# Kernel tuning notes

Hardware: AMD Instinct MI355X
Metric: run time of the kernel (lower is better)

The kernel has to match this reference:

```python
import jax, jax.numpy as jnp
import numpy as np

B, L, H, HEADS = 4, 2048, 512, 8
D = H // HEADS  # 64


def setup_inputs() -> dict:
    key = jax.random.key(0)
    ks = jax.random.split(key, 13)
    s = 0.02
    return {
        "q_in": jax.random.normal(ks[0], (B, L, H), jnp.float32),
        "k_in": jax.random.normal(ks[1], (B, L, H), jnp.float32),
        "v_in": jax.random.normal(ks[2], (B, L, H), jnp.float32),
        "Wq_w": jax.random.normal(ks[3], (H, H), jnp.float32) * s,
        "Wq_b": jax.random.normal(ks[4], (H,), jnp.float32) * s,
        "Wk_w": jax.random.normal(ks[5], (H, H), jnp.float32) * s,
        "Wk_b": jax.random.normal(ks[6], (H,), jnp.float32) * s,
        "Wv_w": jax.random.normal(ks[7], (H, H), jnp.float32) * s,
        "Wv_b": jax.random.normal(ks[8], (H,), jnp.float32) * s,
        "Wo_w": jax.random.normal(ks[9], (H, H), jnp.float32) * s,
        "Wo_b": jax.random.normal(ks[10], (H,), jnp.float32) * s,
        "Wp_w": jax.random.normal(ks[11], (2 * L - 1, D), jnp.float32) * s,
        "Wp_b": jax.random.normal(ks[12], (2 * L - 1,), jnp.float32) * s,
    }


def _skew(p):
    # p: (b, h, l, 2l-1) -> relative-position bias (b, h, l, l) via pad/flatten/reshape skew trick
    b, h, l, _ = p.shape
    p = jnp.pad(p, ((0, 0), (0, 0), (0, 0), (0, 1)))          # (b,h,l,2l)
    p = p.reshape(b, h, 2 * l * l)
    p = jnp.pad(p, ((0, 0), (0, 0), (0, l - 1)))               # (b,h,(l+1)(2l-1))
    p = p.reshape(b, h, l + 1, 2 * l - 1)
    return p[:, :, :-1, -l:]                                   # (b,h,l,l)


def reference(q_in, k_in, v_in, Wq_w, Wq_b, Wk_w, Wk_b, Wv_w, Wv_b, Wo_w, Wo_b, Wp_w, Wp_b):
    b, l, hid = q_in.shape
    q = q_in @ Wq_w.T + Wq_b
    k = k_in @ Wk_w.T + Wk_b
    v = v_in @ Wv_w.T + Wv_b
    # (b, l, h*d) -> (b, h, l, d)
    to_heads = lambda x: x.reshape(b, l, HEADS, D).transpose(0, 2, 1, 3)
    q, k, v = to_heads(q), to_heads(k), to_heads(v)
    q = q / jnp.sqrt(jnp.asarray(D, q.dtype))  # scaling applied BEFORE posenc, as in original
    scores = jnp.einsum('bhid,bhjd->bhij', q, k)
    pos = _skew(q @ Wp_w.T + Wp_b)             # posenc linear applied to scaled q
    scores = scores + pos
    attn = jax.nn.softmax(scores, axis=-1)     # (b,h,l,l)
    # Original torch.einsum('b h l l, b h l d -> b h l d') takes the DIAGONAL of attn
    diag = jnp.diagonal(attn, axis1=-2, axis2=-1)  # (b,h,l)
    out = diag[..., None] * v                       # (b,h,l,d)
    out = out.transpose(0, 2, 1, 3).reshape(b, l, hid)
    return out @ Wo_w.T + Wo_b
```

## Files before the change

### kernel.cpp

```cpp
#include <hip/hip_runtime.h>
#include <cstdint>


typedef unsigned short u16;
typedef __bf16 bf16x8 __attribute__((ext_vector_type(8)));
typedef __bf16 bf16x2 __attribute__((ext_vector_type(2)));
typedef float  f32x16 __attribute__((ext_vector_type(16)));
typedef uint32_t __attribute__((address_space(1))) as1_u32;
typedef uint32_t __attribute__((address_space(3))) as3_u32;

__device__ __forceinline__ u16 f2bf(float f) {
  __bf16 h = (__bf16)f;
  return __builtin_bit_cast(u16, h);
}
__device__ __forceinline__ uint32_t pkbf(float a, float b) {
  bf16x2 v; v[0] = (__bf16)a; v[1] = (__bf16)b;
  return __builtin_bit_cast(uint32_t, v);
}
__device__ __forceinline__ float bf2f(u16 u) {
  return __uint_as_float(((uint32_t)u) << 16);
}
__device__ __forceinline__ float exp2v(float x) {
  float r;
  asm("v_exp_f32 %0, %1" : "=v"(r) : "v"(x));
  return r;
}
__device__ __forceinline__ void gl_lds16(const void* g, void* l) {
  __builtin_amdgcn_global_load_lds((const as1_u32*)g, (as3_u32*)l, 16, 0, 0);
}

__global__ __launch_bounds__(256) void prep_kernel(
    const float* __restrict__ qin, const float* __restrict__ kin, const float* __restrict__ vin,
    const float* __restrict__ wq,  const float* __restrict__ wk,  const float* __restrict__ wv,
    const float* __restrict__ wo,  const float* __restrict__ wp,
    u16* __restrict__ xq, u16* __restrict__ xk, u16* __restrict__ xv,
    u16* __restrict__ bwq, u16* __restrict__ bwk, u16* __restrict__ bwv,
    u16* __restrict__ bwo, u16* __restrict__ bwp) {
  long u = (long)blockIdx.x * 256 + threadIdx.x;
  const float* src; u16* dst; long off; float qs = 1.0f;
  if      (u < 524288L)  { src = qin; dst = xq;  off = u; }
  else if (u < 1048576L) { src = kin; dst = xk;  off = u - 524288L; }
  else if (u < 1572864L) { src = vin; dst = xv;  off = u - 1048576L; }
  else if (u < 1605632L) { src = wq;  dst = bwq; off = u - 1572864L; qs = 0.18033688f; }
  else if (u < 1638400L) { src = wk;  dst = bwk; off = u - 1605632L; }
  else if (u < 1671168L) { src = wv;  dst = bwv; off = u - 1638400L; }
  else if (u < 1703936L) { src = wo;  dst = bwo; off = u - 1671168L; }
  else if (u < 1736696L) { src = wp;  dst = bwp; off = u - 1703936L; }
  else {
    long o = (u - 1736696L) * 8 + 262080L;
    uint4 z = {0u, 0u, 0u, 0u};
    *(uint4*)(bwp + o) = z;
    return;
  }
  const float4* s4 = (const float4*)(src + off * 8);
  float4 a = s4[0], b = s4[1];
  uint32_t p0 = pkbf(a.x * qs, a.y * qs);
  uint32_t p1 = pkbf(a.z * qs, a.w * qs);
  uint32_t p2 = pkbf(b.x * qs, b.y * qs);
  uint32_t p3 = pkbf(b.z * qs, b.w * qs);
  uint4 o = {p0, p1, p2, p3};
  *(uint4*)(dst + off * 8) = o;
}

__device__ __forceinline__ void gemm64_core(
    const u16* __restrict__ A, const u16* __restrict__ W, int m0, int n0,
    u16* Al, u16* Bl, int tid, f32x16& acc) {
  const int lane = tid & 63, w = tid >> 6;
  const int wi = w >> 1, wj = w & 1;
  const int l31 = lane & 31, lh = lane >> 5;
  const int r = tid >> 2, ch = tid & 3;
  const int gch = ch ^ ((r >> 1) & 3);
  for (int kb = 0; kb < 16; ++kb) {
    gl_lds16(A + (long)(m0 + r) * 512 + kb * 32 + gch * 8, (char*)Al + w * 64 * 16);
    gl_lds16(W + (long)(n0 + r) * 512 + kb * 32 + gch * 8, (char*)Bl + w * 64 * 16);
    __syncthreads();
    bf16x8 af[2], bfr[2];
#pragma unroll
    for (int ks = 0; ks < 2; ++ks) {
      int c2 = 2 * ks + lh;
      int rA = 32 * wi + l31;
      int rB = 32 * wj + l31;
      af[ks]  = *(const bf16x8*)((char*)Al + (rA * 4 + (c2 ^ ((rA >> 1) & 3))) * 16);
      bfr[ks] = *(const bf16x8*)((char*)Bl + (rB * 4 + (c2 ^ ((rB >> 1) & 3))) * 16);
    }
#pragma unroll
    for (int ks = 0; ks < 2; ++ks)
      acc = __builtin_amdgcn_mfma_f32_32x32x16_bf16(af[ks], bfr[ks], acc, 0, 0, 0);
    __syncthreads();
  }
}

__global__ __launch_bounds__(256, 4) void gemm_bt(
    const u16* __restrict__ A, const u16* __restrict__ W, const float* __restrict__ bias,
    float* __restrict__ ofp) {
  __shared__ u16 Al[64 * 32];
  __shared__ u16 Bl[64 * 32];
  const int tid = threadIdx.x;
  const int lane = tid & 63, w = tid >> 6;
  const int wi = w >> 1, wj = w & 1;
  const int l31 = lane & 31, lh = lane >> 5;
  const int u = (blockIdx.x & 7) * 128 + (blockIdx.x >> 3);
  const int m0 = (u >> 3) * 64, n0 = (u & 7) * 64;

  float bv = bias[n0 + 32 * wj + l31];
  f32x16 acc;
#pragma unroll
  for (int rr = 0; rr < 16; ++rr) acc[rr] = bv;

  gemm64_core(A, W, m0, n0, Al, Bl, tid, acc);

  int n = n0 + 32 * wj + l31;
#pragma unroll
  for (int rr = 0; rr < 16; ++rr) {
    int row = m0 + 32 * wi + (rr & 3) + 8 * (rr >> 2) + 4 * lh;
    ofp[(long)row * 512 + n] = acc[rr];
  }
}

__global__ __launch_bounds__(256, 4) void qkv_gemm(
    const u16* __restrict__ xq, const u16* __restrict__ xk, const u16* __restrict__ xv,
    const u16* __restrict__ wqp, const u16* __restrict__ wkp, const u16* __restrict__ wvp,
    const float* __restrict__ bq, const float* __restrict__ bk, const float* __restrict__ bv,
    u16* __restrict__ oq, u16* __restrict__ ok, u16* __restrict__ ov) {
  __shared__ u16 Al[64 * 32];
  __shared__ u16 Bl[64 * 32];
  const int mat = blockIdx.x >> 10;
  const int t = blockIdx.x & 1023;
  const u16* A = (mat == 0) ? xq : (mat == 1) ? xk : xv;
  const u16* W = (mat == 0) ? wqp : (mat == 1) ? wkp : wvp;
  const float* bias = (mat == 0) ? bq : (mat == 1) ? bk : bv;
  u16* obf = (mat == 0) ? oq : (mat == 1) ? ok : ov;
  const float bsc = (mat == 0) ? 0.18033688f : 1.0f;

  const int tid = threadIdx.x;
  const int lane = tid & 63, w = tid >> 6;
  const int wi = w >> 1, wj = w & 1;
  const int l31 = lane & 31, lh = lane >> 5;
  const int u = (t & 7) * 128 + (t >> 3);
  const int m0 = (u >> 3) * 64, n0 = (u & 7) * 64;

  float bvv = bias[n0 + 32 * wj + l31] * bsc;
  f32x16 acc;
#pragma unroll
  for (int rr = 0; rr < 16; ++rr) acc[rr] = bvv;

  gemm64_core(A, W, m0, n0, Al, Bl, tid, acc);

  int n = n0 + 32 * wj + l31;
  int h = n >> 6, d = n & 63;
#pragma unroll
  for (int rr = 0; rr < 16; ++rr) {
    int row = m0 + 32 * wi + (rr & 3) + 8 * (rr >> 2) + 4 * lh;
    int b = row >> 11, l = row & 2047;
    obf[(((long)(b * 8 + h)) * 2048 + l) * 64 + d] = f2bf(acc[rr]);
  }
}

#define LOADK(T, K0, K1, K2, K3)                                                 \
  do {                                                                           \
    const u16* kp_ = kb + (long)(c0 + 32 * (T) + l31) * 64 + lh * 8;             \
    K0 = *(const bf16x8*)(kp_);                                                  \
    K1 = *(const bf16x8*)(kp_ + 16);                                             \
    K2 = *(const bf16x8*)(kp_ + 32);                                             \
    K3 = *(const bf16x8*)(kp_ + 48);                                             \
  } while (0)

#define LOADNB(M, N0, N1, N2, N3, NV)                                            \
  do {                                                                           \
    int wr_ = wbA + 32 * (M) + l31;                                              \
    const u16* bp_ = wpw + (long)wr_ * 64 + lh * 8;                              \
    N0 = *(const bf16x8*)(bp_);                                                  \
    N1 = *(const bf16x8*)(bp_ + 16);                                             \
    N2 = *(const bf16x8*)(bp_ + 32);                                             \
    N3 = *(const bf16x8*)(bp_ + 48);                                             \
    NV = wpb[wr_ > 4094 ? 4094 : wr_] * 1.44269504f;                             \
  } while (0)

#define PCOMP(RING, G, AQ0, AQ1, AQ2, AQ3, B0, B1, B2, B3, BV)                   \
  do {                                                                           \
    f32x16 accP;                                                                 \
    _Pragma("unroll")                                                            \
    for (int r = 0; r < 16; ++r) accP[r] = (BV);                                 \
    accP = __builtin_amdgcn_mfma_f32_32x32x16_bf16(AQ0, B0, accP, 0, 0, 0);      \
    accP = __builtin_amdgcn_mfma_f32_32x32x16_bf16(AQ1, B1, accP, 0, 0, 0);      \
    accP = __builtin_amdgcn_mfma_f32_32x32x16_bf16(AQ2, B2, accP, 0, 0, 0);      \
    accP = __builtin_amdgcn_mfma_f32_32x32x16_bf16(AQ3, B3, accP, 0, 0, 0);      \
    int bw_ = 32 * (G) + l31 + 4 * lh;                                           \
    _Pragma("unroll")                                                            \
    for (int r = 0; r < 16; ++r) {                                               \
      const int lrr = (r & 3) + 8 * (r >> 2);                                    \
      int uu = (bw_ + lrr) & 127;                                                \
      (RING)[uu * 38 + lrr + 4 * lh] = f2bf(accP[r]);                            \
    }                                                                            \
  } while (0)

#define GATH(RING, T, ACC)                                                       \
  do {                                                                           \
    int u_ = (31 + l31 + 32 * (T)) & 127;                                        \
    const uint32_t* p_ = (const uint32_t*)((RING) + u_ * 38 + 4 * lh);           \
    uint32_t g0 = p_[0], g1 = p_[1], g2 = p_[4],  g3 = p_[5];                    \
    uint32_t g4 = p_[8], g5 = p_[9], g6 = p_[12], g7 = p_[13];                   \
    ACC[0]  = __uint_as_float(g0 << 16); ACC[1]  = __uint_as_float(g0 & 0xffff0000u); \
    ACC[2]  = __uint_as_float(g1 << 16); ACC[3]  = __uint_as_float(g1 & 0xffff0000u); \
    ACC[4]  = __uint_as_float(g2 << 16); ACC[5]  = __uint_as_float(g2 & 0xffff0000u); \
    ACC[6]  = __uint_as_float(g3 << 16); ACC[7]  = __uint_as_float(g3 & 0xffff0000u); \
    ACC[8]  = __uint_as_float(g4 << 16); ACC[9]  = __uint_as_float(g4 & 0xffff0000u); \
    ACC[10] = __uint_as_float(g5 << 16); ACC[11] = __uint_as_float(g5 & 0xffff0000u); \
    ACC[12] = __uint_as_float(g6 << 16); ACC[13] = __uint_as_float(g6 & 0xffff0000u); \
    ACC[14] = __uint_as_float(g7 << 16); ACC[15] = __uint_as_float(g7 & 0xffff0000u); \
  } while (0)

#define ATTN_STEP(T, KC0, KC1, KC2, KC3, KN0, KN1, KN2, KN3,                     \
                  NU0, NU1, NU2, NU3, NUV, NN0, NN1, NN2, NN3, NNV,              \
                  DOK, DOP)                                                      \
  do {                                                                           \
    const int t_ = (T);                                                          \
    if (DOK) { LOADK(t_ + 1, KN0, KN1, KN2, KN3); }                              \
    if (DOP) { LOADNB(t_ + 2, NN0, NN1, NN2, NN3, NNV); }                        \
    accSA = __builtin_amdgcn_mfma_f32_32x32x16_bf16(aqA0, KC0, accSA, 0, 0, 0);  \
    accSA = __builtin_amdgcn_mfma_f32_32x32x16_bf16(aqA1, KC1, accSA, 0, 0, 0);  \
    accSA = __builtin_amdgcn_mfma_f32_32x32x16_bf16(aqA2, KC2, accSA, 0, 0, 0);  \
    accSA = __builtin_amdgcn_mfma_f32_32x32x16_bf16(aqA3, KC3, accSA, 0, 0, 0);  \
    accSB = __builtin_amdgcn_mfma_f32_32x32x16_bf16(aqB0, KC0, accSB, 0, 0, 0);  \
    accSB = __builtin_amdgcn_mfma_f32_32x32x16_bf16(aqB1, KC1, accSB, 0, 0, 0);  \
    accSB = __builtin_amdgcn_mfma_f32_32x32x16_bf16(aqB2, KC2, accSB, 0, 0, 0);  \
    accSB = __builtin_amdgcn_mfma_f32_32x32x16_bf16(aqB3, KC3, accSB, 0, 0, 0);  \
    if (diagw && t_ == tdA) {                                                    \
      _Pragma("unroll")                                                          \
      for (int r = 0; r < 16; ++r) {                                             \
        const int lrr = (r & 3) + 8 * (r >> 2);                                  \
        if (l31 == lrr + 4 * lh) sdiag[lrr + 4 * lh] = accSA[r];                 \
      }                                                                          \
    }                                                                            \
    if (diagw && t_ == tdA + 1) {                                                \
      _Pragma("unroll")                                                          \
      for (int r = 0; r < 16; ++r) {                                             \
        const int lrr = (r & 3) + 8 * (r >> 2);                                  \
        if (l31 == lrr + 4 * lh) sdiag[32 + lrr + 4 * lh] = accSB[r];            \
      }                                                                          \
    }                                                                            \
    _Pragma("unroll")                                                            \
    for (int r = 0; r < 16; ++r) rsum[r] += exp2v(accSA[r]);                     \
    _Pragma("unroll")                                                            \
    for (int r = 0; r < 16; ++r) rsum[16 + r] += exp2v(accSB[r]);                \
    if (DOP) {                                                                   \
      PCOMP(ringB, t_ + 2, aqB0, aqB1, aqB2, aqB3, NU0, NU1, NU2, NU3, NUV);     \
      PCOMP(ringA, t_ + 2, aqA0, aqA1, aqA2, aqA3, NN0, NN1, NN2, NN3, NNV);     \
      GATH(ringA, t_ + 1, accSA);                                                \
      GATH(ringB, t_ + 1, accSB);                                                \
    }                                                                            \
  } while (0)

__global__ __launch_bounds__(256, 2) void attn_kernel(
    const u16* __restrict__ qw, const u16* __restrict__ kw, const u16* __restrict__ vw,
    const u16* __restrict__ wpw, const float* __restrict__ wpb, u16* __restrict__ outp) {
  __shared__ u16 Pl[8 * 128 * 38];
  __shared__ float sdiag[64];
  __shared__ float rssum[64 * 4];
  __shared__ float attw[64];

  const int tid = threadIdx.x, lane = tid & 63, w = tid >> 6;
  const int sbi = blockIdx.x;
  const int x = sbi & 7, g = sbi >> 3;
  const int bh = x + 8 * (g >> 5);
  const int it = g & 31;
  const int i0 = it * 64;
  const u16* qb = qw + (long)bh * 2048 * 64;
  const u16* kb = kw + (long)bh * 2048 * 64;
  const u16* vb = vw + (long)bh * 2048 * 64;

  const int l31 = lane & 31, lh = lane >> 5;
  const int c0 = w << 9;
  const int wbA = 2016 + c0 - i0;
  const bool diagw = (w == (it >> 3));
  const int tdA = 2 * (it & 7);

  u16* ringA = Pl + w * 9728;
  u16* ringB = ringA + 4864;

  bf16x8 aqA0, aqA1, aqA2, aqA3, aqB0, aqB1, aqB2, aqB3;
  {
    const u16* pA = qb + (long)(i0 + l31) * 64 + lh * 8;
    aqA0 = *(const bf16x8*)(pA);
    aqA1 = *(const bf16x8*)(pA + 16);
    aqA2 = *(const bf16x8*)(pA + 32);
    aqA3 = *(const bf16x8*)(pA + 48);
    const u16* pB = pA + 32 * 64;
    aqB0 = *(const bf16x8*)(pB);
    aqB1 = *(const bf16x8*)(pB + 16);
    aqB2 = *(const bf16x8*)(pB + 32);
    aqB3 = *(const bf16x8*)(pB + 48);
  }

  float rsum[32];
#pragma unroll
  for (int r = 0; r < 32; ++r) rsum[r] = 0.f;

  bf16x8 kfA0, kfA1, kfA2, kfA3, kfB0, kfB1, kfB2, kfB3;
  bf16x8 nb00, nb01, nb02, nb03, nb10, nb11, nb12, nb13;
  float nbv0, nbv1;
  f32x16 accSA, accSB;

  {
    bf16x8 t0, t1, t2, t3; float tv;
    LOADNB(-1, t0, t1, t2, t3, tv);
    PCOMP(ringB, 0, aqB0, aqB1, aqB2, aqB3, t0, t1, t2, t3, tv);
    LOADNB(0, t0, t1, t2, t3, tv);
    PCOMP(ringA, 0, aqA0, aqA1, aqA2, aqA3, t0, t1, t2, t3, tv);
    PCOMP(ringB, 1, aqB0, aqB1, aqB2, aqB3, t0, t1, t2, t3, tv);
    LOADNB(1, nb10, nb11, nb12, nb13, nbv1);
    PCOMP(ringA, 1, aqA0, aqA1, aqA2, aqA3, nb10, nb11, nb12, nb13, nbv1);
    LOADK(0, kfA0, kfA1, kfA2, kfA3);
    GATH(ringA, 0, accSA);
    GATH(ringB, 0, accSB);
  }

  for (int tt = 0; tt < 14; tt += 2) {
    ATTN_STEP(tt,     kfA0, kfA1, kfA2, kfA3, kfB0, kfB1, kfB2, kfB3,
              nb10, nb11, nb12, nb13, nbv1, nb00, nb01, nb02, nb03, nbv0,
              true, true);
    ATTN_STEP(tt + 1, kfB0, kfB1, kfB2, kfB3, kfA0, kfA1, kfA2, kfA3,
              nb00, nb01, nb02, nb03, nbv0, nb10, nb11, nb12, nb13, nbv1,
              true, true);
  }
  ATTN_STEP(14, kfA0, kfA1, kfA2, kfA3, kfB0, kfB1, kfB2, kfB3,
            nb10, nb11, nb12, nb13, nbv1, nb00, nb01, nb02, nb03, nbv0,
            true, true);
  ATTN_STEP(15, kfB0, kfB1, kfB2, kfB3, kfA0, kfA1, kfA2, kfA3,
            nb00, nb01, nb02, nb03, nbv0, nb10, nb11, nb12, nb13, nbv1,
            false, false);

#pragma unroll
  for (int r = 0; r < 32; ++r) {
    float v = rsum[r];
    v += __shfl_xor(v, 1);
    v += __shfl_xor(v, 2);
    v += __shfl_xor(v, 4);
    v += __shfl_xor(v, 8);
    v += __shfl_xor(v, 16);
    rsum[r] = v;
  }
  if (l31 == 0) {
#pragma unroll
    for (int r = 0; r < 16; ++r) {
      int lr = (r & 3) + 8 * (r >> 2) + 4 * lh;
      rssum[lr * 4 + w] = rsum[r];
      rssum[(32 + lr) * 4 + w] = rsum[16 + r];
    }
  }
  __syncthreads();
  if (tid < 64) {
    float S = rssum[tid * 4] + rssum[tid * 4 + 1] + rssum[tid * 4 + 2] + rssum[tid * 4 + 3];
    attw[tid] = exp2v(sdiag[tid]) / S;
  }
  __syncthreads();
  {
    int r = tid >> 2, dd = (tid & 3) * 16;
    float a = attw[r];
    int b = bh >> 3, h = bh & 7;
    const u16* vp = vb + (long)(i0 + r) * 64 + dd;
    u16* op = outp + ((long)(b * 2048 + i0 + r)) * 512 + h * 64 + dd;
    uint4 v0 = *(const uint4*)vp;
    uint4 v1 = *(const uint4*)(vp + 8);
    uint32_t vin[8] = {v0.x, v0.y, v0.z, v0.w, v1.x, v1.y, v1.z, v1.w};
    uint32_t vout[8];
#pragma unroll
    for (int e = 0; e < 8; ++e) {
      float lo = bf2f((u16)(vin[e] & 0xffffu)) * a;
      float hi = bf2f((u16)(vin[e] >> 16)) * a;
      vout[e] = pkbf(lo, hi);
    }
    uint4 o0 = {vout[0], vout[1], vout[2], vout[3]};
    uint4 o1 = {vout[4], vout[5], vout[6], vout[7]};
    *(uint4*)op = o0;
    *(uint4*)(op + 8) = o1;
  }
}

extern "C" void kernel_launch(void* const* d_in, const int* in_sizes, int n_in,
                              void* d_out, int out_size, void* d_ws, size_t ws_size,
                              hipStream_t stream) {
  (void)in_sizes; (void)n_in; (void)out_size; (void)ws_size;
  const float* q_in = (const float*)d_in[0];
  const float* k_in = (const float*)d_in[1];
  const float* v_in = (const float*)d_in[2];
  const float* Wq_w = (const float*)d_in[3];
  const float* Wq_b = (const float*)d_in[4];
  const float* Wk_w = (const float*)d_in[5];
  const float* Wk_b = (const float*)d_in[6];
  const float* Wv_w = (const float*)d_in[7];
  const float* Wv_b = (const float*)d_in[8];
  const float* Wo_w = (const float*)d_in[9];
  const float* Wo_b = (const float*)d_in[10];
  const float* Wp_w = (const float*)d_in[11];
  const float* Wp_b = (const float*)d_in[12];

  char* ws = (char*)d_ws;
  u16* xq    = (u16*)(ws + 0);
  u16* xk    = (u16*)(ws + 8388608);
  u16* xv    = (u16*)(ws + 16777216);
  u16* wq    = (u16*)(ws + 25165824);
  u16* wk    = (u16*)(ws + 25690112);
  u16* wv    = (u16*)(ws + 26214400);
  u16* wo    = (u16*)(ws + 26738688);
  u16* wp    = (u16*)(ws + 27262976);
  u16* q_ws  = (u16*)(ws + 27787264);
  u16* k_ws  = (u16*)(ws + 36175872);
  u16* v_ws  = (u16*)(ws + 44564480);
  u16* opre  = (u16*)(ws + 52953088);

  prep_kernel<<<6784, 256, 0, stream>>>(q_in, k_in, v_in, Wq_w, Wk_w, Wv_w, Wo_w, Wp_w,
                                        xq, xk, xv, wq, wk, wv, wo, wp);
  qkv_gemm<<<3072, 256, 0, stream>>>(xq, xk, xv, wq, wk, wv, Wq_b, Wk_b, Wv_b,
                                     q_ws, k_ws, v_ws);
  attn_kernel<<<1024, 256, 0, stream>>>(q_ws, k_ws, v_ws, wp, Wp_b, opre);
  gemm_bt<<<1024, 256, 0, stream>>>(opre, wo, Wo_b, (float*)d_out);
}
```

Baseline: 229.6 us.

## Deepen attention positional-bias pipeline and load GEMM operands directly from global

The attention loop now computes the positional-bias tiles three steps ahead instead of two. The ring gather is split into an early LDS load and a later unpack, so the LDS reads overlap the exp/sum work of the next step. Separately, the projection GEMMs drop the LDS staging and the two barriers per k-step, and each wave loads its bf16 fragments straight from global memory in a fully unrolled loop. This trades barrier and LDS overhead for redundant global traffic across waves and higher register pressure from the deeper prefetch.

Result: slower. 305.7 us (+33.2%).

```diff
diff --git a/kernel.cpp b/kernel.cpp
--- a/kernel.cpp
+++ b/kernel.cpp
@@ -24,9 +24,6 @@
   float r;
   asm("v_exp_f32 %0, %1" : "=v"(r) : "v"(x));
   return r;
-}
-__device__ __forceinline__ void gl_lds16(const void* g, void* l) {
-  __builtin_amdgcn_global_load_lds((const as1_u32*)g, (as3_u32*)l, 16, 0, 0);
 }
 
 __global__ __launch_bounds__(256) void prep_kernel(
@@ -62,39 +59,25 @@
   *(uint4*)(dst + off * 8) = o;
 }
 
-__device__ __forceinline__ void gemm64_core(
+__device__ __forceinline__ void gemm64_direct(
     const u16* __restrict__ A, const u16* __restrict__ W, int m0, int n0,
-    u16* Al, u16* Bl, int tid, f32x16& acc) {
-  const int lane = tid & 63, w = tid >> 6;
-  const int wi = w >> 1, wj = w & 1;
-  const int l31 = lane & 31, lh = lane >> 5;
-  const int r = tid >> 2, ch = tid & 3;
-  const int gch = ch ^ ((r >> 1) & 3);
+    int wi, int wj, int l31, int lh, f32x16& acc) {
+  const u16* Ap = A + (long)(m0 + 32 * wi + l31) * 512 + lh * 8;
+  const u16* Wp = W + (long)(n0 + 32 * wj + l31) * 512 + lh * 8;
+#pragma unroll
   for (int kb = 0; kb < 16; ++kb) {
-    gl_lds16(A + (long)(m0 + r) * 512 + kb * 32 + gch * 8, (char*)Al + w * 64 * 16);
-    gl_lds16(W + (long)(n0 + r) * 512 + kb * 32 + gch * 8, (char*)Bl + w * 64 * 16);
-    __syncthreads();
-    bf16x8 af[2], bfr[2];
-#pragma unroll
-    for (int ks = 0; ks < 2; ++ks) {
-      int c2 = 2 * ks + lh;
-      int rA = 32 * wi + l31;
-      int rB = 32 * wj + l31;
-      af[ks]  = *(const bf16x8*)((char*)Al + (rA * 4 + (c2 ^ ((rA >> 1) & 3))) * 16);
-      bfr[ks] = *(const bf16x8*)((char*)Bl + (rB * 4 + (c2 ^ ((rB >> 1) & 3))) * 16);
-    }
-#pragma unroll
-    for (int ks = 0; ks < 2; ++ks)
-      acc = __builtin_amdgcn_mfma_f32_32x32x16_bf16(af[ks], bfr[ks], acc, 0, 0, 0);
-    __syncthreads();
+    bf16x8 a0 = *(const bf16x8*)(Ap + kb * 32);
+    bf16x8 a1 = *(const bf16x8*)(Ap + kb * 32 + 16);
+    bf16x8 b0 = *(const bf16x8*)(Wp + kb * 32);
+    bf16x8 b1 = *(const bf16x8*)(Wp + kb * 32 + 16);
+    acc = __builtin_amdgcn_mfma_f32_32x32x16_bf16(a0, b0, acc, 0, 0, 0);
+    acc = __builtin_amdgcn_mfma_f32_32x32x16_bf16(a1, b1, acc, 0, 0, 0);
   }
 }
 
 __global__ __launch_bounds__(256, 4) void gemm_bt(
     const u16* __restrict__ A, const u16* __restrict__ W, const float* __restrict__ bias,
     float* __restrict__ ofp) {
-  __shared__ u16 Al[64 * 32];
-  __shared__ u16 Bl[64 * 32];
   const int tid = threadIdx.x;
   const int lane = tid & 63, w = tid >> 6;
   const int wi = w >> 1, wj = w & 1;
@@ -107,7 +90,7 @@
 #pragma unroll
   for (int rr = 0; rr < 16; ++rr) acc[rr] = bv;
 
-  gemm64_core(A, W, m0, n0, Al, Bl, tid, acc);
+  gemm64_direct(A, W, m0, n0, wi, wj, l31, lh, acc);
 
   int n = n0 + 32 * wj + l31;
 #pragma unroll
@@ -122,8 +105,6 @@
     const u16* __restrict__ wqp, const u16* __restrict__ wkp, const u16* __restrict__ wvp,
     const float* __restrict__ bq, const float* __restrict__ bk, const float* __restrict__ bv,
     u16* __restrict__ oq, u16* __restrict__ ok, u16* __restrict__ ov) {
-  __shared__ u16 Al[64 * 32];
-  __shared__ u16 Bl[64 * 32];
   const int mat = blockIdx.x >> 10;
   const int t = blockIdx.x & 1023;
   const u16* A = (mat == 0) ? xq : (mat == 1) ? xk : xv;
@@ -144,7 +125,7 @@
 #pragma unroll
   for (int rr = 0; rr < 16; ++rr) acc[rr] = bvv;
 
-  gemm64_core(A, W, m0, n0, Al, Bl, tid, acc);
+  gemm64_direct(A, W, m0, n0, wi, wj, l31, lh, acc);
 
   int n = n0 + 32 * wj + l31;
   int h = n >> 6, d = n & 63;
@@ -194,29 +175,36 @@
     }                                                                            \
   } while (0)
 
-#define GATH(RING, T, ACC)                                                       \
+#define GATH_ISSUE(RING, T, G0, G1, G2, G3, G4, G5, G6, G7)                      \
   do {                                                                           \
     int u_ = (31 + l31 + 32 * (T)) & 127;                                        \
     const uint32_t* p_ = (const uint32_t*)((RING) + u_ * 38 + 4 * lh);           \
-    uint32_t g0 = p_[0], g1 = p_[1], g2 = p_[4],  g3 = p_[5];                    \
-    uint32_t g4 = p_[8], g5 = p_[9], g6 = p_[12], g7 = p_[13];                   \
-    ACC[0]  = __uint_as_float(g0 << 16); ACC[1]  = __uint_as_float(g0 & 0xffff0000u); \
-    ACC[2]  = __uint_as_float(g1 << 16); ACC[3]  = __uint_as_float(g1 & 0xffff0000u); \
-    ACC[4]  = __uint_as_float(g2 << 16); ACC[5]  = __uint_as_float(g2 & 0xffff0000u); \
-    ACC[6]  = __uint_as_float(g3 << 16); ACC[7]  = __uint_as_float(g3 & 0xffff0000u); \
-    ACC[8]  = __uint_as_float(g4 << 16); ACC[9]  = __uint_as_float(g4 & 0xffff0000u); \
-    ACC[10] = __uint_as_float(g5 << 16); ACC[11] = __uint_as_float(g5 & 0xffff0000u); \
-    ACC[12] = __uint_as_float(g6 << 16); ACC[13] = __uint_as_float(g6 & 0xffff0000u); \
-    ACC[14] = __uint_as_float(g7 << 16); ACC[15] = __uint_as_float(g7 & 0xffff0000u); \
+    G0 = p_[0]; G1 = p_[1]; G2 = p_[4];  G3 = p_[5];                             \
+    G4 = p_[8]; G5 = p_[9]; G6 = p_[12]; G7 = p_[13];                            \
+  } while (0)
+
+#define UNPACK(G0, G1, G2, G3, G4, G5, G6, G7, ACC)                              \
+  do {                                                                           \
+    ACC[0]  = __uint_as_float(G0 << 16); ACC[1]  = __uint_as_float(G0 & 0xffff0000u); \
+    ACC[2]  = __uint_as_float(G1 << 16); ACC[3]  = __uint_as_float(G1 & 0xffff0000u); \
+    ACC[4]  = __uint_as_float(G2 << 16); ACC[5]  = __uint_as_float(G2 & 0xffff0000u); \
+    ACC[6]  = __uint_as_float(G3 << 16); ACC[7]  = __uint_as_float(G3 & 0xffff0000u); \
+    ACC[8]  = __uint_as_float(G4 << 16); ACC[9]  = __uint_as_float(G4 & 0xffff0000u); \
+    ACC[10] = __uint_as_float(G5 << 16); ACC[11] = __uint_as_float(G5 & 0xffff0000u); \
+    ACC[12] = __uint_as_float(G6 << 16); ACC[13] = __uint_as_float(G6 & 0xffff0000u); \
+    ACC[14] = __uint_as_float(G7 << 16); ACC[15] = __uint_as_float(G7 & 0xffff0000u); \
   } while (0)
 
 #define ATTN_STEP(T, KC0, KC1, KC2, KC3, KN0, KN1, KN2, KN3,                     \
                   NU0, NU1, NU2, NU3, NUV, NN0, NN1, NN2, NN3, NNV,              \
-                  DOK, DOP)                                                      \
+                  DOK, DONB, DOG, DOP)                                           \
   do {                                                                           \
     const int t_ = (T);                                                          \
     if (DOK) { LOADK(t_ + 1, KN0, KN1, KN2, KN3); }                              \
-    if (DOP) { LOADNB(t_ + 2, NN0, NN1, NN2, NN3, NNV); }                        \
+    if (DONB) { LOADNB(t_ + 3, NN0, NN1, NN2, NN3, NNV); }                       \
+    f32x16 accSA, accSB;                                                         \
+    UNPACK(gA0, gA1, gA2, gA3, gA4, gA5, gA6, gA7, accSA);                       \
+    UNPACK(gB0, gB1, gB2, gB3, gB4, gB5, gB6, gB7, accSB);                       \
     accSA = __builtin_amdgcn_mfma_f32_32x32x16_bf16(aqA0, KC0, accSA, 0, 0, 0);  \
     accSA = __builtin_amdgcn_mfma_f32_32x32x16_bf16(aqA1, KC1, accSA, 0, 0, 0);  \
     accSA = __builtin_amdgcn_mfma_f32_32x32x16_bf16(aqA2, KC2, accSA, 0, 0, 0);  \
@@ -243,11 +231,13 @@
     for (int r = 0; r < 16; ++r) rsum[r] += exp2v(accSA[r]);                     \
     _Pragma("unroll")                                                            \
     for (int r = 0; r < 16; ++r) rsum[16 + r] += exp2v(accSB[r]);                \
+    if (DOG) {                                                                   \
+      GATH_ISSUE(ringA, t_ + 1, gA0, gA1, gA2, gA3, gA4, gA5, gA6, gA7);         \
+      GATH_ISSUE(ringB, t_ + 1, gB0, gB1, gB2, gB3, gB4, gB5, gB6, gB7);         \
+    }                                                                            \
     if (DOP) {                                                                   \
-      PCOMP(ringB, t_ + 2, aqB0, aqB1, aqB2, aqB3, NU0, NU1, NU2, NU3, NUV);     \
-      PCOMP(ringA, t_ + 2, aqA0, aqA1, aqA2, aqA3, NN0, NN1, NN2, NN3, NNV);     \
-      GATH(ringA, t_ + 1, accSA);                                                \
-      GATH(ringB, t_ + 1, accSB);                                                \
+      PCOMP(ringB, t_ + 3, aqB0, aqB1, aqB2, aqB3, NU0, NU1, NU2, NU3, NUV);     \
+      PCOMP(ringA, t_ + 3, aqA0, aqA1, aqA2, aqA3, NN0, NN1, NN2, NN3, NNV);     \
     }                                                                            \
   } while (0)
 
@@ -299,7 +289,8 @@
   bf16x8 kfA0, kfA1, kfA2, kfA3, kfB0, kfB1, kfB2, kfB3;
   bf16x8 nb00, nb01, nb02, nb03, nb10, nb11, nb12, nb13;
   float nbv0, nbv1;
-  f32x16 accSA, accSB;
+  uint32_t gA0, gA1, gA2, gA3, gA4, gA5, gA6, gA7;
+  uint32_t gB0, gB1, gB2, gB3, gB4, gB5, gB6, gB7;
 
   {
     bf16x8 t0, t1, t2, t3; float tv;
@@ -308,27 +299,36 @@
     LOADNB(0, t0, t1, t2, t3, tv);
     PCOMP(ringA, 0, aqA0, aqA1, aqA2, aqA3, t0, t1, t2, t3, tv);
     PCOMP(ringB, 1, aqB0, aqB1, aqB2, aqB3, t0, t1, t2, t3, tv);
-    LOADNB(1, nb10, nb11, nb12, nb13, nbv1);
-    PCOMP(ringA, 1, aqA0, aqA1, aqA2, aqA3, nb10, nb11, nb12, nb13, nbv1);
+    LOADNB(1, t0, t1, t2, t3, tv);
+    PCOMP(ringA, 1, aqA0, aqA1, aqA2, aqA3, t0, t1, t2, t3, tv);
+    PCOMP(ringB, 2, aqB0, aqB1, aqB2, aqB3, t0, t1, t2, t3, tv);
+    LOADNB(2, nb10, nb11, nb12, nb13, nbv1);
+    PCOMP(ringA, 2, aqA0, aqA1, aqA2, aqA3, nb10, nb11, nb12, nb13, nbv1);
     LOADK(0, kfA0, kfA1, kfA2, kfA3);
-    GATH(ringA, 0, accSA);
-    GATH(ringB, 0, accSB);
-  }
-
-  for (int tt = 0; tt < 14; tt += 2) {
+    GATH_ISSUE(ringA, 0, gA0, gA1, gA2, gA3, gA4, gA5, gA6, gA7);
+    GATH_ISSUE(ringB, 0, gB0, gB1, gB2, gB3, gB4, gB5, gB6, gB7);
+  }
+
+  for (int tt = 0; tt < 12; tt += 2) {
     ATTN_STEP(tt,     kfA0, kfA1, kfA2, kfA3, kfB0, kfB1, kfB2, kfB3,
               nb10, nb11, nb12, nb13, nbv1, nb00, nb01, nb02, nb03, nbv0,
-              true, true);
+              true, true, true, true);
     ATTN_STEP(tt + 1, kfB0, kfB1, kfB2, kfB3, kfA0, kfA1, kfA2, kfA3,
               nb00, nb01, nb02, nb03, nbv0, nb10, nb11, nb12, nb13, nbv1,
-              true, true);
-  }
+              true, true, true, true);
+  }
+  ATTN_STEP(12, kfA0, kfA1, kfA2, kfA3, kfB0, kfB1, kfB2, kfB3,
+            nb10, nb11, nb12, nb13, nbv1, nb00, nb01, nb02, nb03, nbv0,
+            true, true, true, true);
+  ATTN_STEP(13, kfB0, kfB1, kfB2, kfB3, kfA0, kfA1, kfA2, kfA3,
+            nb00, nb01, nb02, nb03, nbv0, nb10, nb11, nb12, nb13, nbv1,
+            true, false, true, true);
   ATTN_STEP(14, kfA0, kfA1, kfA2, kfA3, kfB0, kfB1, kfB2, kfB3,
             nb10, nb11, nb12, nb13, nbv1, nb00, nb01, nb02, nb03, nbv0,
-            true, true);
+            true, false, true, false);
   ATTN_STEP(15, kfB0, kfB1, kfB2, kfB3, kfA0, kfA1, kfA2, kfA3,
             nb00, nb01, nb02, nb03, nbv0, nb10, nb11, nb12, nb13, nbv1,
-            false, false);
+            false, false, false, false);
 
 #pragma unroll
   for (int r = 0; r < 32; ++r) {
```
